# Kernel tuning notes

Hardware: AMD Instinct MI355X
Metric: run time of the kernel (lower is better)

Reference implementation:

```python
import jax, jax.numpy as jnp
import numpy as np

S, IN, H, D, B, BOT, IMG, TXT = 4, 4096, 2048, 6, 1024, 128, 768, 768


def _gelu(x):
    # torch nn.GELU default = exact erf gelu
    return jax.nn.gelu(x, approximate=False)


def _ln(x, g, b, eps=1e-5):
    mu = jnp.mean(x, axis=-1, keepdims=True)
    var = jnp.mean(jnp.square(x - mu), axis=-1, keepdims=True)
    return g * (x - mu) / jnp.sqrt(var + eps) + b


def setup_inputs() -> dict:
    key = jax.random.key(0)
    ks = jax.random.split(key, 16)
    n = lambda k, shp, s=0.02: jax.random.normal(k, shp, dtype=jnp.float32) * s
    return dict(
        voxels=jax.random.normal(ks[0], (B, IN), dtype=jnp.float32),
        subject_ids=jax.random.randint(ks[1], (B,), 0, S, dtype=jnp.int32),
        # per-subject encoder params, stacked on leading subject axis S
        ad_down_w=n(ks[2], (S, IN, BOT)), ad_down_b=n(ks[3], (S, BOT)),
        ad_up_w=n(ks[4], (S, BOT, IN)), ad_up_b=n(ks[5], (S, IN)),
        enc_w=n(ks[6], (S, IN, H)), enc_b=n(ks[7], (S, H)),
        enc_ln_g=jnp.ones((S, H), jnp.float32), enc_ln_b=jnp.zeros((S, H), jnp.float32),
        # shared ResidualStack params, stacked on leading depth axis D
        bb_w=n(ks[8], (D, H, H)), bb_b=n(ks[9], (D, H)),
        bb_ln_g=jnp.ones((D, H), jnp.float32), bb_ln_b=jnp.zeros((D, H), jnp.float32),
        # heads
        img_w=n(ks[10], (H, IMG)), img_b=n(ks[11], (IMG,)),
        txt_w=n(ks[12], (H, TXT)), txt_b=n(ks[13], (TXT,)),
    )


def _forward(voxels, subject_ids, ad_down_w, ad_down_b, ad_up_w, ad_up_b,
             enc_w, enc_b, enc_ln_g, enc_ln_b, bb_w, bb_b, bb_ln_g, bb_ln_b,
             img_w, img_b, txt_w, txt_b):
    # --- subject-routed encoders (dense dispatch over the small fixed subject set) ---
    def enc_one(dw, db, uw, ub, ew, eb, g, be):
        # BottleneckAdapter: x + up(gelu(down(x)))
        h = voxels + _gelu(voxels @ dw + db) @ uw + ub          # [B, IN]
        # Linear -> LayerNorm -> GELU (Dropout is identity in eval)
        return _gelu(_ln(h @ ew + eb, g, be))                    # [B, H]

    feats_all = jax.vmap(enc_one)(ad_down_w, ad_down_b, ad_up_w, ad_up_b,
                                  enc_w, enc_b, enc_ln_g, enc_ln_b)  # [S, B, H]
    x = feats_all[subject_ids, jnp.arange(voxels.shape[0])]          # [B, H] pick own subject

    # --- shared ResidualStack: x = x + gelu(ln(linear(x))) per block ---
    def step(x, p):
        w, b, g, be = p
        return x + _gelu(_ln(x @ w + b, g, be)), None

    x, _ = jax.lax.scan(step, x, (bb_w, bb_b, bb_ln_g, bb_ln_b))

    return x @ img_w + img_b, x @ txt_w + txt_b  # (image_embedding, text_embedding)


def reference(voxels, subject_ids, ad_down_w, ad_down_b, ad_up_w, ad_up_b,
              enc_w, enc_b, enc_ln_g, enc_ln_b, bb_w, bb_b, bb_ln_g, bb_ln_b,
              img_w, img_b, txt_w, txt_b):
    return _forward(voxels, subject_ids, ad_down_w, ad_down_b, ad_up_w, ad_up_b,
                    enc_w, enc_b, enc_ln_g, enc_ln_b, bb_w, bb_b, bb_ln_g, bb_ln_b,
                    img_w, img_b, txt_w, txt_b)
```

## Files before the change

kernel.cpp:

```cpp
#include <hip/hip_runtime.h>
#include <hip/hip_bf16.h>
#include <stdint.h>

typedef __bf16 bf16x8 __attribute__((ext_vector_type(8)));
typedef float  f32x4  __attribute__((ext_vector_type(4)));

#define DEV __device__ __forceinline__

constexpr int SUBJ  = 4;
constexpr int IN    = 4096;
constexpr int H     = 2048;
constexpr int DEPTH = 6;
constexpr int BATCH = 1024;
constexpr int BOT   = 128;
constexpr int IMG   = 768;
constexpr int TXT   = 768;
constexpr int MP    = 1408;
constexpr int MT    = 11;

DEV float gelu_exact(float x){ return 0.5f*x*(1.0f + erff(x*0.70710678118654752440f)); }

DEV uint16_t bf16_bits(float x){
  __hip_bfloat16 h = __float2bfloat16(x);
  return *reinterpret_cast<uint16_t*>(&h);
}

struct CvtSeg { const float* src; size_t dst_off; };
struct CvtParams { CvtSeg s[6]; size_t total_items; };

__global__ void convert_weights(CvtParams p, __hip_bfloat16* __restrict__ dst){
  size_t stride = (size_t)gridDim.x * blockDim.x;
  for (size_t it = (size_t)blockIdx.x*blockDim.x + threadIdx.x; it < p.total_items; it += stride){
    size_t e = it << 3;
    int si = 0;
    #pragma unroll
    for (int i = 1; i < 6; ++i) if (e >= p.s[i].dst_off) si = i;
    const float* s = p.s[si].src + (e - p.s[si].dst_off);
    float4 a = *reinterpret_cast<const float4*>(s);
    float4 b = *reinterpret_cast<const float4*>(s + 4);
    uint16_t o[8] = {bf16_bits(a.x), bf16_bits(a.y), bf16_bits(a.z), bf16_bits(a.w),
                     bf16_bits(b.x), bf16_bits(b.y), bf16_bits(b.z), bf16_bits(b.w)};
    *reinterpret_cast<uint4*>(dst + e) = *reinterpret_cast<const uint4*>(o);
  }
}

__global__ void sort_kernel(const int* __restrict__ ids, int* __restrict__ rowmap,
                            int* __restrict__ tileS){
  __shared__ int hist[16][4];
  __shared__ int basew[16][4];
  __shared__ int pstart[5];
  int tid = threadIdx.x;
  if (tid < MP) rowmap[tid] = -1;
  if (tid + 1024 < MP) rowmap[tid + 1024] = -1;
  int w = tid >> 6, lane = tid & 63;
  int my = ids[tid];
  unsigned long long mymask = 0ull;
  #pragma unroll
  for (int s = 0; s < 4; ++s){
    unsigned long long m = __ballot(my == s);
    if (lane == 0) hist[w][s] = (int)__popcll(m);
    if (s == my) mymask = m;
  }
  int myrank = (int)__popcll(mymask & ((1ull << lane) - 1ull));
  __syncthreads();
  if (tid == 0){
    for (int s = 0; s < 4; ++s){
      int run = 0;
      for (int ww = 0; ww < 16; ++ww){ basew[ww][s] = run; run += hist[ww][s]; }
      hist[0][s] = run;
    }
    pstart[0] = 0;
    for (int s = 0; s < 4; ++s) pstart[s+1] = pstart[s] + ((hist[0][s] + 127) & ~127);
  }
  __syncthreads();
  int pos = pstart[my] + basew[w][my] + myrank;
  rowmap[pos] = tid;
  if (tid < MT){
    int row0 = tid << 7, s = -1;
    for (int ss = 0; ss < 4; ++ss) if (row0 >= pstart[ss] && row0 < pstart[ss+1]) s = ss;
    tileS[tid] = s;
  }
}

__global__ void gather_voxels(const float* __restrict__ vox, const int* __restrict__ rowmap,
                              __hip_bfloat16* __restrict__ Vs){
  int r = blockIdx.x, tid = threadIdx.x;
  int orig = rowmap[r];
  #pragma unroll
  for (int i = 0; i < 4; ++i){
    int c = (i*256 + tid) << 2;
    float4 v = {0.f,0.f,0.f,0.f};
    if (orig >= 0) v = *reinterpret_cast<const float4*>(vox + (size_t)orig*IN + c);
    __hip_bfloat16 o[4] = {__float2bfloat16(v.x), __float2bfloat16(v.y),
                           __float2bfloat16(v.z), __float2bfloat16(v.w)};
    *reinterpret_cast<uint2*>(Vs + (size_t)r*IN + c) = *reinterpret_cast<const uint2*>(o);
  }
}

enum { EPI_SPLIT = 0, EPI_RES_BF16 = 1, EPI_HEADS = 3 };

template<int EPI, int TAG>
__global__ __launch_bounds__(256, 2)
void gemm_bf16(const __hip_bfloat16* __restrict__ A, int lda,
               const __hip_bfloat16* __restrict__ Bw, int ldn, long long wsub,
               const int* __restrict__ tileS, const int* __restrict__ rowmap,
               int nx, int qnt, int ksplit,
               const float* __restrict__ bias, int biassub,
               const float* __restrict__ resid, int ldres,
               float* __restrict__ outf, __hip_bfloat16* __restrict__ outb, int ldo,
               size_t pstride, const __hip_bfloat16* __restrict__ Bw2)
{
  int b   = blockIdx.x;
  int xcd = b & 7;
  int r0  = b >> 3;
  int mt  = r0 % MT;
  int q   = r0 / MT;
  int kzi = xcd / nx + (q / qnt) * (8 / nx);
  int nt  = (q % qnt) * nx + (xcd % nx);

  int s = tileS[mt];
  if (s < 0) return;
  const __hip_bfloat16* Ab = A + (size_t)mt*128*lda;

  const __hip_bfloat16* Bb;
  int ntl = nt;
  if constexpr (EPI == EPI_HEADS){
    if (nt < 6){ Bb = Bw  + (size_t)nt*128; }
    else       { Bb = Bw2 + (size_t)(nt-6)*128; }
    ntl = nt;
  } else {
    Bb = Bw + (size_t)s*wsub + (size_t)nt*128;
  }

  int kb = kzi * ksplit;
  int nk = ksplit >> 6;

  __shared__ __hip_bfloat16 sA[2][128*64];
  __shared__ __hip_bfloat16 sB[2][128*64];

  int tid = threadIdx.x;
  int lane = tid & 63;
  int wv = tid >> 6, wr = wv >> 1, wc = wv & 1;

  int kq = tid >> 5;
  int nq = tid & 31;
  int n4 = nq << 2;

  f32x4 acc[4][4];
  #pragma unroll
  for (int i = 0; i < 4; ++i)
    #pragma unroll
    for (int j = 0; j < 4; ++j) acc[i][j] = (f32x4){0.f,0.f,0.f,0.f};

  auto stageA = [&](int buf, int k0){
    #pragma unroll
    for (int i = 0; i < 4; ++i){
      int cell = i*256 + tid;
      int row = cell >> 3, cc = cell & 7;
      int kg = k0 + ((cc ^ (row & 7)) << 3);
      __builtin_amdgcn_global_load_lds(
        (const __attribute__((address_space(1))) void*)(Ab + (size_t)row*lda + kg),
        (__attribute__((address_space(3))) void*)(&sA[buf][cell<<3]), 16, 0, 0);
    }
  };

  auto stageB_load = [&](int k0g, uint2* F){
    const __hip_bfloat16* p = Bb + (size_t)(k0g + (kq<<3))*ldn + n4;
    #pragma unroll
    for (int rr = 0; rr < 8; ++rr)
      F[rr] = *reinterpret_cast<const uint2*>(p + (size_t)rr*ldn);
  };
  auto stageB_write = [&](int buf, const uint2* F){
    #pragma unroll
    for (int j = 0; j < 4; ++j){
      int n = n4 + j;
      int cell = (kq ^ (n >> 3) ^ n) & 7;
      auto US = [&](int rr)->uint32_t{
        return (((const uint32_t*)&F[rr])[j >> 1] >> ((j & 1) * 16)) & 0xffffu;
      };
      uint4 d;
      d.x = US(0) | (US(1) << 16);
      d.y = US(2) | (US(3) << 16);
      d.z = US(4) | (US(5) << 16);
      d.w = US(6) | (US(7) << 16);
      *reinterpret_cast<uint4*>(&sB[buf][(n<<6) + (cell<<3)]) = d;
    }
  };

  uint2 F[8];
  stageB_load(kb, F);
  stageA(0, kb);
  stageB_write(0, F);
  __syncthreads();

  for (int t = 0; t < nk; ++t){
    if (t+1 < nk){
      stageB_load(kb + ((t+1)<<6), F);
      stageA((t+1)&1, kb + ((t+1)<<6));
    }
    const char* baseA = (const char*)(&sA[t&1][0]);
    const char* baseB = (const char*)(&sB[t&1][0]);
    int rA = (wr<<6) + (lane & 15);
    int rB = (wc<<6) + (lane & 15);
    #pragma unroll
    for (int kk = 0; kk < 2; ++kk){
      int koffA = ((((kk<<5) + ((lane>>4)<<3)) << 1)) ^ ((lane & 7) << 4);
      bf16x8 av[4], bv[4];
      #pragma unroll
      for (int f = 0; f < 4; ++f){
        int rowA = rA + f*16;
        av[f] = *reinterpret_cast<const bf16x8*>(baseA + (size_t)rowA*128 + koffA);
        int rowB = rB + f*16;
        int cellB = (((kk<<2) + (lane>>4)) ^ (rowB >> 3) ^ rowB) & 7;
        bv[f] = *reinterpret_cast<const bf16x8*>(baseB + (size_t)rowB*128 + (cellB<<4));
      }
      #pragma unroll
      for (int i = 0; i < 4; ++i)
        #pragma unroll
        for (int j = 0; j < 4; ++j)
          acc[i][j] = __builtin_amdgcn_mfma_f32_16x16x32_bf16(av[i], bv[j], acc[i][j], 0, 0, 0);
    }
    if (t+1 < nk) stageB_write((t+1)&1, F);
    __syncthreads();
  }

  #pragma unroll
  for (int i = 0; i < 4; ++i){
    int rbase = (mt<<7) + (wr<<6) + (i<<4) + ((lane>>4)<<2);
    #pragma unroll
    for (int j = 0; j < 4; ++j){
      int colp = (wc<<6) + (j<<4) + (lane & 15);
      #pragma unroll
      for (int qq = 0; qq < 4; ++qq){
        int r = rbase + qq;
        float v = acc[i][j][qq];
        if constexpr (EPI == EPI_SPLIT){
          int col = (nt<<7) + colp;
          outf[(size_t)kzi*pstride + (size_t)r*ldo + col] = v;
        } else if constexpr (EPI == EPI_RES_BF16){
          int col = (nt<<7) + colp;
          int orig = rowmap[r];
          if (orig >= 0){
            v += bias[(size_t)s*biassub + col] + resid[(size_t)orig*ldres + col];
            outb[(size_t)r*ldo + col] = __float2bfloat16(v);
          }
        } else {
          int col = (ntl<<7) + colp;
          outf[(size_t)kzi*pstride + (size_t)r*ldo + col] = v;
        }
      }
    }
  }
}

template<int NPART>
__global__ void t1_epilogue(const float* __restrict__ Tp, const float* __restrict__ db,
                            const int* __restrict__ rowmap, const int* __restrict__ tileS,
                            __hip_bfloat16* __restrict__ T1){
  int idx = blockIdx.x*256 + threadIdx.x;
  int r = idx >> 7, c = idx & 127;
  float v = 0.f;
  if (rowmap[r] >= 0){
    int s = tileS[r >> 7];
    float acc = 0.f;
    #pragma unroll
    for (int p = 0; p < NPART; ++p) acc += Tp[(size_t)p*MP*BOT + idx];
    v = gelu_exact(acc + db[s*BOT + c]);
  }
  T1[idx] = __float2bfloat16(v);
}

template<int RES, int NPART>
__global__ void ln_gelu_kernel(const float* __restrict__ Zp, size_t pstride,
                               const float* __restrict__ g,
                               const float* __restrict__ b, int gsub,
                               const float* __restrict__ lb,
                               const int* __restrict__ tileS, const int* __restrict__ rowmap,
                               float* __restrict__ Xf, __hip_bfloat16* __restrict__ Xb){
  int r = blockIdx.x, tid = threadIdx.x;
  size_t rowoff = (size_t)r * H;
  int c0 = tid << 3;
  int orig = rowmap[r];
  if (orig < 0){
    float4 zf = {0.f,0.f,0.f,0.f};
    *reinterpret_cast<float4*>(Xf + rowoff + c0)     = zf;
    *reinterpret_cast<float4*>(Xf + rowoff + c0 + 4) = zf;
    uint4 zu = {0u,0u,0u,0u};
    *reinterpret_cast<uint4*>(Xb + rowoff + c0) = zu;
    return;
  }
  int si = gsub ? tileS[r>>7] : 0;
  const float* gp  = g  + (size_t)si*gsub;
  const float* bp  = b  + (size_t)si*gsub;
  const float* lbp = lb + (size_t)si*gsub;
  float z[8];
  #pragma unroll
  for (int j = 0; j < 8; ++j) z[j] = lbp[c0+j];
  #pragma unroll
  for (int p = 0; p < NPART; ++p){
    float4 v1 = *reinterpret_cast<const float4*>(Zp + p*pstride + rowoff + c0);
    float4 v2 = *reinterpret_cast<const float4*>(Zp + p*pstride + rowoff + c0 + 4);
    z[0]+=v1.x; z[1]+=v1.y; z[2]+=v1.z; z[3]+=v1.w;
    z[4]+=v2.x; z[5]+=v2.y; z[6]+=v2.z; z[7]+=v2.w;
  }
  float s1 = 0.f, s2 = 0.f;
  #pragma unroll
  for (int j = 0; j < 8; ++j){ s1 += z[j]; s2 += z[j]*z[j]; }
  #pragma unroll
  for (int m = 32; m >= 1; m >>= 1){ s1 += __shfl_xor(s1, m); s2 += __shfl_xor(s2, m); }
  __shared__ float red[4][2];
  int wv = tid >> 6, lane = tid & 63;
  if (lane == 0){ red[wv][0] = s1; red[wv][1] = s2; }
  __syncthreads();
  s1 = red[0][0]+red[1][0]+red[2][0]+red[3][0];
  s2 = red[0][1]+red[1][1]+red[2][1]+red[3][1];
  const float invH = 1.f / (float)H;
  float mu  = s1 * invH;
  float var = s2 * invH - mu*mu;
  float rs  = rsqrtf(var + 1e-5f);
  float o[8];
  #pragma unroll
  for (int j = 0; j < 8; ++j){
    float t = (z[j]-mu)*rs*gp[c0+j] + bp[c0+j];
    o[j] = gelu_exact(t);
  }
  if constexpr (RES){
    float4 x1 = *reinterpret_cast<const float4*>(Xf + rowoff + c0);
    float4 x2 = *reinterpret_cast<const float4*>(Xf + rowoff + c0 + 4);
    o[0]+=x1.x; o[1]+=x1.y; o[2]+=x1.z; o[3]+=x1.w;
    o[4]+=x2.x; o[5]+=x2.y; o[6]+=x2.z; o[7]+=x2.w;
  }
  float4 w1 = {o[0],o[1],o[2],o[3]}, w2 = {o[4],o[5],o[6],o[7]};
  *reinterpret_cast<float4*>(Xf + rowoff + c0)     = w1;
  *reinterpret_cast<float4*>(Xf + rowoff + c0 + 4) = w2;
  __hip_bfloat16 ob[8];
  #pragma unroll
  for (int j = 0; j < 8; ++j) ob[j] = __float2bfloat16(o[j]);
  *reinterpret_cast<uint4*>(Xb + rowoff + c0) = *reinterpret_cast<const uint4*>(ob);
}

__global__ void head_combine(const float* __restrict__ Hp, size_t pstride,
                             const float* __restrict__ img_b, const float* __restrict__ txt_b,
                             const int* __restrict__ rowmap,
                             float* __restrict__ oimg, float* __restrict__ otxt){
  int r = blockIdx.x;
  int orig = rowmap[r];
  if (orig < 0) return;
  int col = threadIdx.x << 2;
  size_t base = (size_t)r*(IMG+TXT) + col;
  float4 v0 = *reinterpret_cast<const float4*>(Hp + base);
  float4 v1 = *reinterpret_cast<const float4*>(Hp + pstride + base);
  float4 bb = (col < IMG)
            ? *reinterpret_cast<const float4*>(img_b + col)
            : *reinterpret_cast<const float4*>(txt_b + (col - IMG));
  float4 o = {v0.x+v1.x+bb.x, v0.y+v1.y+bb.y, v0.z+v1.z+bb.z, v0.w+v1.w+bb.w};
  if (col < IMG) *reinterpret_cast<float4*>(oimg + (size_t)orig*IMG + col) = o;
  else           *reinterpret_cast<float4*>(otxt + (size_t)orig*TXT + (col-IMG)) = o;
}

extern "C" void kernel_launch(void* const* d_in, const int* in_sizes, int n_in,
                              void* d_out, int out_size, void* d_ws, size_t ws_size,
                              hipStream_t stream){
  (void)in_sizes; (void)n_in; (void)out_size; (void)ws_size;
  const float* vox       = (const float*)d_in[0];
  const int*   ids       = (const int*)  d_in[1];
  const float* ad_down_w = (const float*)d_in[2];
  const float* ad_down_b = (const float*)d_in[3];
  const float* ad_up_w   = (const float*)d_in[4];
  const float* ad_up_b   = (const float*)d_in[5];
  const float* enc_w     = (const float*)d_in[6];
  const float* enc_b     = (const float*)d_in[7];
  const float* enc_ln_g  = (const float*)d_in[8];
  const float* enc_ln_bb = (const float*)d_in[9];
  const float* bb_w      = (const float*)d_in[10];
  const float* bb_b      = (const float*)d_in[11];
  const float* bb_ln_g   = (const float*)d_in[12];
  const float* bb_ln_b   = (const float*)d_in[13];
  const float* img_w     = (const float*)d_in[14];
  const float* img_b     = (const float*)d_in[15];
  const float* txt_w     = (const float*)d_in[16];
  const float* txt_b     = (const float*)d_in[17];
  float* out = (float*)d_out;

  const size_t N_DOWN = (size_t)SUBJ*IN*BOT;
  const size_t N_UP   = (size_t)SUBJ*BOT*IN;
  const size_t N_ENC  = (size_t)SUBJ*IN*H;
  const size_t N_BB   = (size_t)DEPTH*H*H;
  const size_t N_IMG  = (size_t)H*IMG;
  const size_t N_TXT  = (size_t)H*TXT;

  char* wp = (char*)d_ws;
  auto alloc = [&](size_t bytes)->char*{ char* p = wp; wp += (bytes + 255) & ~(size_t)255; return p; };
  int* rowmap = (int*)alloc(MP * sizeof(int));
  int* tileS  = (int*)alloc(MT * sizeof(int));
  __hip_bfloat16* Wbf = (__hip_bfloat16*)alloc((N_DOWN+N_UP+N_ENC+N_BB+N_IMG+N_TXT)*2);
  __hip_bfloat16* w_down = Wbf;
  __hip_bfloat16* w_up   = w_down + N_DOWN;
  __hip_bfloat16* w_enc  = w_up   + N_UP;
  __hip_bfloat16* w_bb   = w_enc  + N_ENC;
  __hip_bfloat16* w_img  = w_bb   + N_BB;
  __hip_bfloat16* w_txt  = w_img  + N_IMG;
  __hip_bfloat16* Vs    = (__hip_bfloat16*)alloc((size_t)MP*IN*2);
  float* T1p            = (float*)alloc((size_t)16*MP*BOT*4);
  __hip_bfloat16* T1    = (__hip_bfloat16*)alloc((size_t)MP*BOT*2);
  __hip_bfloat16* Hs    = (__hip_bfloat16*)alloc((size_t)MP*IN*2);
  float* Zp             = (float*)alloc((size_t)4*MP*H*4);
  float* Hp             = Zp;
  float* Xf             = (float*)alloc((size_t)MP*H*4);
  __hip_bfloat16* Xb    = (__hip_bfloat16*)alloc((size_t)MP*H*2);

  const size_t ZPS = (size_t)MP*H;
  const size_t TPS = (size_t)MP*BOT;
  const size_t HPS = (size_t)MP*(IMG+TXT);

  CvtParams cp;
  size_t off = 0;
  cp.s[0] = {ad_down_w, off}; off += N_DOWN;
  cp.s[1] = {ad_up_w,   off}; off += N_UP;
  cp.s[2] = {enc_w,     off}; off += N_ENC;
  cp.s[3] = {bb_w,      off}; off += N_BB;
  cp.s[4] = {img_w,     off}; off += N_IMG;
  cp.s[5] = {txt_w,     off}; off += N_TXT;
  cp.total_items = off >> 3;
  convert_weights<<<2048, 256, 0, stream>>>(cp, Wbf);

  sort_kernel<<<1, 1024, 0, stream>>>(ids, rowmap, tileS);
  gather_voxels<<<MP, 256, 0, stream>>>(vox, rowmap, Vs);

  gemm_bf16<EPI_SPLIT,1><<<MT*16, 256, 0, stream>>>(
      Vs, IN, w_down, BOT, (long long)IN*BOT, tileS, rowmap, 1, 1, 256,
      nullptr, 0, nullptr, 0, T1p, nullptr, BOT, TPS, nullptr);
  t1_epilogue<16><<<MP*BOT/256, 256, 0, stream>>>(T1p, ad_down_b, rowmap, tileS, T1);

  gemm_bf16<EPI_RES_BF16,2><<<MT*32, 256, 0, stream>>>(
      T1, BOT, w_up, IN, (long long)BOT*IN, tileS, rowmap, 8, 4, 128,
      ad_up_b, IN, vox, IN, nullptr, Hs, IN, 0, nullptr);

  gemm_bf16<EPI_SPLIT,3><<<MT*8*8, 256, 0, stream>>>(
      Hs, IN, w_enc, H, (long long)IN*H, tileS, rowmap, 2, 8, 1024,
      nullptr, 0, nullptr, 0, Zp, nullptr, H, ZPS, nullptr);
  ln_gelu_kernel<0,4><<<MP, 256, 0, stream>>>(Zp, ZPS, enc_ln_g, enc_ln_bb, H, enc_b,
                                              tileS, rowmap, Xf, Xb);

  for (int d = 0; d < DEPTH; ++d){
    gemm_bf16<EPI_SPLIT,4><<<MT*4*8, 256, 0, stream>>>(
        Xb, H, w_bb + (size_t)d*H*H, H, 0, tileS, rowmap, 4, 4, 1024,
        nullptr, 0, nullptr, 0, Zp, nullptr, H, ZPS, nullptr);
    ln_gelu_kernel<1,2><<<MP, 256, 0, stream>>>(Zp, ZPS, bb_ln_g + (size_t)d*H,
                                                bb_ln_b + (size_t)d*H, 0, bb_b + (size_t)d*H,
                                                tileS, rowmap, Xf, Xb);
  }

  gemm_bf16<EPI_HEADS,5><<<MT*3*8, 256, 0, stream>>>(
      Xb, H, w_img, IMG, 0, tileS, rowmap, 4, 3, 1024,
      nullptr, 0, nullptr, 0, Hp, nullptr, IMG+TXT, HPS, w_txt);
  head_combine<<<MP, 384, 0, stream>>>(Hp, HPS, img_b, txt_b, rowmap,
                                       out, out + (size_t)BATCH*IMG);
}
```

Baseline: 470.9 us.

## Store split-K GEMM partials in bf16 and widen weight conversion per thread

Split-K partial sums from every GEMM (down-projection, encoder, residual blocks, heads) are now written as bf16 rather than fp32. The reducing kernels (t1 epilogue, LN+GELU, head combine) read bf16 and widen it to fp32, which halves partial-buffer traffic. The weight-conversion kernel now handles 32 elements per thread in a single pass over an exact grid, replacing the grid-stride loop of 8. This adds rounding error to each partial before reduction, which can hurt accuracy, especially with 16 partials for the bottleneck.

```diff
diff --git a/kernel.cpp b/kernel.cpp
--- a/kernel.cpp
+++ b/kernel.cpp
@@ -24,24 +24,35 @@
   __hip_bfloat16 h = __float2bfloat16(x);
   return *reinterpret_cast<uint16_t*>(&h);
 }
+DEV float bfu(uint32_t w, int hi){
+  uint32_t x = hi ? (w & 0xffff0000u) : (w << 16);
+  return __uint_as_float(x);
+}
+DEV float bf2f(uint16_t u){ uint32_t x = (uint32_t)u << 16; return __uint_as_float(x); }
 
 struct CvtSeg { const float* src; size_t dst_off; };
 struct CvtParams { CvtSeg s[6]; size_t total_items; };
 
 __global__ void convert_weights(CvtParams p, __hip_bfloat16* __restrict__ dst){
-  size_t stride = (size_t)gridDim.x * blockDim.x;
-  for (size_t it = (size_t)blockIdx.x*blockDim.x + threadIdx.x; it < p.total_items; it += stride){
-    size_t e = it << 3;
-    int si = 0;
-    #pragma unroll
-    for (int i = 1; i < 6; ++i) if (e >= p.s[i].dst_off) si = i;
-    const float* s = p.s[si].src + (e - p.s[si].dst_off);
-    float4 a = *reinterpret_cast<const float4*>(s);
-    float4 b = *reinterpret_cast<const float4*>(s + 4);
-    uint16_t o[8] = {bf16_bits(a.x), bf16_bits(a.y), bf16_bits(a.z), bf16_bits(a.w),
-                     bf16_bits(b.x), bf16_bits(b.y), bf16_bits(b.z), bf16_bits(b.w)};
-    *reinterpret_cast<uint4*>(dst + e) = *reinterpret_cast<const uint4*>(o);
-  }
+  size_t it = (size_t)blockIdx.x*blockDim.x + threadIdx.x;
+  if (it >= p.total_items) return;
+  size_t e = it << 5;
+  int si = 0;
+  #pragma unroll
+  for (int i = 1; i < 6; ++i) if (e >= p.s[i].dst_off) si = i;
+  const float* s = p.s[si].src + (e - p.s[si].dst_off);
+  float4 f[8];
+  #pragma unroll
+  for (int i = 0; i < 8; ++i) f[i] = *reinterpret_cast<const float4*>(s + 4*i);
+  uint16_t o[32];
+  #pragma unroll
+  for (int i = 0; i < 8; ++i){
+    o[4*i+0] = bf16_bits(f[i].x); o[4*i+1] = bf16_bits(f[i].y);
+    o[4*i+2] = bf16_bits(f[i].z); o[4*i+3] = bf16_bits(f[i].w);
+  }
+  #pragma unroll
+  for (int i = 0; i < 4; ++i)
+    *reinterpret_cast<uint4*>(dst + e + 8*i) = *reinterpret_cast<const uint4*>(&o[8*i]);
 }
 
 __global__ void sort_kernel(const int* __restrict__ ids, int* __restrict__ rowmap,
@@ -107,7 +118,7 @@
                int nx, int qnt, int ksplit,
                const float* __restrict__ bias, int biassub,
                const float* __restrict__ resid, int ldres,
-               float* __restrict__ outf, __hip_bfloat16* __restrict__ outb, int ldo,
+               __hip_bfloat16* __restrict__ outb, int ldo,
                size_t pstride, const __hip_bfloat16* __restrict__ Bw2)
 {
   int b   = blockIdx.x;
@@ -236,7 +247,7 @@
         float v = acc[i][j][qq];
         if constexpr (EPI == EPI_SPLIT){
           int col = (nt<<7) + colp;
-          outf[(size_t)kzi*pstride + (size_t)r*ldo + col] = v;
+          outb[(size_t)kzi*pstride + (size_t)r*ldo + col] = __float2bfloat16(v);
         } else if constexpr (EPI == EPI_RES_BF16){
           int col = (nt<<7) + colp;
           int orig = rowmap[r];
@@ -246,7 +257,7 @@
           }
         } else {
           int col = (ntl<<7) + colp;
-          outf[(size_t)kzi*pstride + (size_t)r*ldo + col] = v;
+          outb[(size_t)kzi*pstride + (size_t)r*ldo + col] = __float2bfloat16(v);
         }
       }
     }
@@ -254,7 +265,7 @@
 }
 
 template<int NPART>
-__global__ void t1_epilogue(const float* __restrict__ Tp, const float* __restrict__ db,
+__global__ void t1_epilogue(const __hip_bfloat16* __restrict__ Tp, const float* __restrict__ db,
                             const int* __restrict__ rowmap, const int* __restrict__ tileS,
                             __hip_bfloat16* __restrict__ T1){
   int idx = blockIdx.x*256 + threadIdx.x;
@@ -264,14 +275,15 @@
     int s = tileS[r >> 7];
     float acc = 0.f;
     #pragma unroll
-    for (int p = 0; p < NPART; ++p) acc += Tp[(size_t)p*MP*BOT + idx];
+    for (int p = 0; p < NPART; ++p)
+      acc += bf2f(*reinterpret_cast<const uint16_t*>(Tp + (size_t)p*MP*BOT + idx));
     v = gelu_exact(acc + db[s*BOT + c]);
   }
   T1[idx] = __float2bfloat16(v);
 }
 
 template<int RES, int NPART>
-__global__ void ln_gelu_kernel(const float* __restrict__ Zp, size_t pstride,
+__global__ void ln_gelu_kernel(const __hip_bfloat16* __restrict__ Zp, size_t pstride,
                                const float* __restrict__ g,
                                const float* __restrict__ b, int gsub,
                                const float* __restrict__ lb,
@@ -298,10 +310,11 @@
   for (int j = 0; j < 8; ++j) z[j] = lbp[c0+j];
   #pragma unroll
   for (int p = 0; p < NPART; ++p){
-    float4 v1 = *reinterpret_cast<const float4*>(Zp + p*pstride + rowoff + c0);
-    float4 v2 = *reinterpret_cast<const float4*>(Zp + p*pstride + rowoff + c0 + 4);
-    z[0]+=v1.x; z[1]+=v1.y; z[2]+=v1.z; z[3]+=v1.w;
-    z[4]+=v2.x; z[5]+=v2.y; z[6]+=v2.z; z[7]+=v2.w;
+    uint4 v = *reinterpret_cast<const uint4*>(Zp + p*pstride + rowoff + c0);
+    z[0] += bfu(v.x,0); z[1] += bfu(v.x,1);
+    z[2] += bfu(v.y,0); z[3] += bfu(v.y,1);
+    z[4] += bfu(v.z,0); z[5] += bfu(v.z,1);
+    z[6] += bfu(v.w,0); z[7] += bfu(v.w,1);
   }
   float s1 = 0.f, s2 = 0.f;
   #pragma unroll
@@ -339,7 +352,7 @@
   *reinterpret_cast<uint4*>(Xb + rowoff + c0) = *reinterpret_cast<const uint4*>(ob);
 }
 
-__global__ void head_combine(const float* __restrict__ Hp, size_t pstride,
+__global__ void head_combine(const __hip_bfloat16* __restrict__ Hp, size_t pstride,
                              const float* __restrict__ img_b, const float* __restrict__ txt_b,
                              const int* __restrict__ rowmap,
                              float* __restrict__ oimg, float* __restrict__ otxt){
@@ -348,12 +361,17 @@
   if (orig < 0) return;
   int col = threadIdx.x << 2;
   size_t base = (size_t)r*(IMG+TXT) + col;
-  float4 v0 = *reinterpret_cast<const float4*>(Hp + base);
-  float4 v1 = *reinterpret_cast<const float4*>(Hp + pstride + base);
+  uint2 u0 = *reinterpret_cast<const uint2*>(Hp + base);
+  uint2 u1 = *reinterpret_cast<const uint2*>(Hp + pstride + base);
+  float4 acc;
+  acc.x = bfu(u0.x,0) + bfu(u1.x,0);
+  acc.y = bfu(u0.x,1) + bfu(u1.x,1);
+  acc.z = bfu(u0.y,0) + bfu(u1.y,0);
+  acc.w = bfu(u0.y,1) + bfu(u1.y,1);
   float4 bb = (col < IMG)
             ? *reinterpret_cast<const float4*>(img_b + col)
             : *reinterpret_cast<const float4*>(txt_b + (col - IMG));
-  float4 o = {v0.x+v1.x+bb.x, v0.y+v1.y+bb.y, v0.z+v1.z+bb.z, v0.w+v1.w+bb.w};
+  float4 o = {acc.x+bb.x, acc.y+bb.y, acc.z+bb.z, acc.w+bb.w};
   if (col < IMG) *reinterpret_cast<float4*>(oimg + (size_t)orig*IMG + col) = o;
   else           *reinterpret_cast<float4*>(otxt + (size_t)orig*TXT + (col-IMG)) = o;
 }
@@ -401,11 +419,11 @@
   __hip_bfloat16* w_img  = w_bb   + N_BB;
   __hip_bfloat16* w_txt  = w_img  + N_IMG;
   __hip_bfloat16* Vs    = (__hip_bfloat16*)alloc((size_t)MP*IN*2);
-  float* T1p            = (float*)alloc((size_t)16*MP*BOT*4);
+  __hip_bfloat16* T1p   = (__hip_bfloat16*)alloc((size_t)16*MP*BOT*2);
   __hip_bfloat16* T1    = (__hip_bfloat16*)alloc((size_t)MP*BOT*2);
   __hip_bfloat16* Hs    = (__hip_bfloat16*)alloc((size_t)MP*IN*2);
-  float* Zp             = (float*)alloc((size_t)4*MP*H*4);
-  float* Hp             = Zp;
+  __hip_bfloat16* Zp    = (__hip_bfloat16*)alloc((size_t)4*MP*H*2);
+  __hip_bfloat16* Hp    = Zp;
   float* Xf             = (float*)alloc((size_t)MP*H*4);
   __hip_bfloat16* Xb    = (__hip_bfloat16*)alloc((size_t)MP*H*2);
 
@@ -421,31 +439,32 @@
   cp.s[3] = {bb_w,      off}; off += N_BB;
   cp.s[4] = {img_w,     off}; off += N_IMG;
   cp.s[5] = {txt_w,     off}; off += N_TXT;
-  cp.total_items = off >> 3;
-  convert_weights<<<2048, 256, 0, stream>>>(cp, Wbf);
+  cp.total_items = off >> 5;
+  int cvt_blocks = (int)((cp.total_items + 255) / 256);
+  convert_weights<<<cvt_blocks, 256, 0, stream>>>(cp, Wbf);
 
   sort_kernel<<<1, 1024, 0, stream>>>(ids, rowmap, tileS);
   gather_voxels<<<MP, 256, 0, stream>>>(vox, rowmap, Vs);
 
   gemm_bf16<EPI_SPLIT,1><<<MT*16, 256, 0, stream>>>(
       Vs, IN, w_down, BOT, (long long)IN*BOT, tileS, rowmap, 1, 1, 256,
-      nullptr, 0, nullptr, 0, T1p, nullptr, BOT, TPS, nullptr);
+      nullptr, 0, nullptr, 0, T1p, BOT, TPS, nullptr);
   t1_epilogue<16><<<MP*BOT/256, 256, 0, stream>>>(T1p, ad_down_b, rowmap, tileS, T1);
 
   gemm_bf16<EPI_RES_BF16,2><<<MT*32, 256, 0, stream>>>(
       T1, BOT, w_up, IN, (long long)BOT*IN, tileS, rowmap, 8, 4, 128,
-      ad_up_b, IN, vox, IN, nullptr, Hs, IN, 0, nullptr);
+      ad_up_b, IN, vox, IN, Hs, IN, 0, nullptr);
 
   gemm_bf16<EPI_SPLIT,3><<<MT*8*8, 256, 0, stream>>>(
       Hs, IN, w_enc, H, (long long)IN*H, tileS, rowmap, 2, 8, 1024,
-      nullptr, 0, nullptr, 0, Zp, nullptr, H, ZPS, nullptr);
+      nullptr, 0, nullptr, 0, Zp, H, ZPS, nullptr);
   ln_gelu_kernel<0,4><<<MP, 256, 0, stream>>>(Zp, ZPS, enc_ln_g, enc_ln_bb, H, enc_b,
                                               tileS, rowmap, Xf, Xb);
 
   for (int d = 0; d < DEPTH; ++d){
     gemm_bf16<EPI_SPLIT,4><<<MT*4*8, 256, 0, stream>>>(
         Xb, H, w_bb + (size_t)d*H*H, H, 0, tileS, rowmap, 4, 4, 1024,
-        nullptr, 0, nullptr, 0, Zp, nullptr, H, ZPS, nullptr);
+        nullptr, 0, nullptr, 0, Zp, H, ZPS, nullptr);
     ln_gelu_kernel<1,2><<<MP, 256, 0, stream>>>(Zp, ZPS, bb_ln_g + (size_t)d*H,
                                                 bb_ln_b + (size_t)d*H, 0, bb_b + (size_t)d*H,
                                                 tileS, rowmap, Xf, Xb);
@@ -453,7 +472,7 @@
 
   gemm_bf16<EPI_HEADS,5><<<MT*3*8, 256, 0, stream>>>(
       Xb, H, w_img, IMG, 0, tileS, rowmap, 4, 3, 1024,
-      nullptr, 0, nullptr, 0, Hp, nullptr, IMG+TXT, HPS, w_txt);
+      nullptr, 0, nullptr, 0, Hp, IMG+TXT, HPS, w_txt);
   head_combine<<<MP, 384, 0, stream>>>(Hp, HPS, img_b, txt_b, rowmap,
                                        out, out + (size_t)BATCH*IMG);
 }
```

Result: no change. 461.6 us (-2.0%).
